# Optimization experiments

Measured on AMD Instinct MI355X. Metric: run time of the kernel, lower is better.

## Reference

```python
import jax, jax.numpy as jnp
import numpy as np

# Constants describing the (equal-length) ragged batch and CRF tag space
B, L = 64, 512                 # 64 sequences of 512 segment-tokens each
C = 1024                       # fuse_embedding_channel
NUM_CLASSES = 5                # real field classes
NUM_TAGS = NUM_CLASSES + 2     # + START + STOP
START, STOP = NUM_CLASSES, NUM_CLASSES + 1
NEG = -10000.0


def setup_inputs() -> dict:
    key = jax.random.key(0)
    k1, k2, k3, k4 = jax.random.split(key, 4)
    fuse_embeddings = jax.random.normal(k1, (B * L, C), jnp.float32)
    label_class = jax.random.randint(k2, (B * L,), 0, NUM_CLASSES)
    # classification head params (Linear C -> NUM_TAGS)
    W = jax.random.normal(k3, (NUM_TAGS, C), jnp.float32) * 0.02
    b = jnp.zeros((NUM_TAGS,), jnp.float32)
    # CRF transition matrix: transitions[next, prev]
    transitions = jax.random.normal(k4, (NUM_TAGS, NUM_TAGS), jnp.float32) * 0.01
    transitions = transitions.at[START, :].set(NEG).at[:, STOP].set(NEG)
    return {"fuse_embeddings": fuse_embeddings, "label_class": label_class,
            "W": W, "b": b, "transitions": transitions}


def _crf_nll_sum(feats, tags, transitions):
    """Sum over batch of (forward_alg score - gold score).
    feats: [B, L, T] emissions, tags: [B, L] int, transitions: [T, T] (next, prev)."""
    # --- forward algorithm (batched log-sum-exp recurrence) ---
    init = jnp.full((B, NUM_TAGS), NEG, feats.dtype).at[:, START].set(0.0)

    def step(fv, emit):
        # fv: [B, prev], emit: [B, next]
        fv_new = jax.nn.logsumexp(fv[:, None, :] + transitions[None, :, :], axis=2) + emit
        return fv_new, None

    fv, _ = jax.lax.scan(step, init, jnp.swapaxes(feats, 0, 1))  # scan over L
    fwd_score = jax.nn.logsumexp(fv + transitions[STOP][None, :], axis=1)  # [B]

    # --- gold sentence score ---
    tags_ext = jnp.concatenate([jnp.full((B, 1), START, tags.dtype), tags], axis=1)
    emit_sc = jnp.take_along_axis(feats, tags[..., None], axis=2)[..., 0].sum(axis=1)
    trans_sc = transitions[tags_ext[:, 1:], tags_ext[:, :-1]].sum(axis=1)
    gold = emit_sc + trans_sc + transitions[STOP, tags[:, -1]]
    return (fwd_score - gold).sum()


def reference(fuse_embeddings, label_class, W, b, transitions):
    # per-token linear projection to tag logits
    pred_class = fuse_embeddings @ W.T + b          # [N, NUM_TAGS]
    feats = pred_class.reshape(B, L, NUM_TAGS)
    tags = label_class.reshape(B, L)
    score = _crf_nll_sum(feats, tags, transitions)
    return (jnp.reshape(score, (1,)), label_class.astype(jnp.int32), pred_class)
```

## Files before the change

### kernel.cpp

```cpp
#include <hip/hip_runtime.h>

#define BSEQ 64
#define LSEQ 512
#define CCH  1024
#define NT   7
#define NC   5
#define NTOK (BSEQ*LSEQ)
#define START_TAG 5
#define STOP_TAG  6
#define NEGV (-10000.0f)
#define GRID_LOGITS 1024

typedef float vfloat4 __attribute__((ext_vector_type(4)));

template<int CTRL, int RMASK, int BMASK>
__device__ __forceinline__ float dpp_add(float x) {
    int y = __builtin_amdgcn_update_dpp(0, __float_as_int(x), CTRL, RMASK, BMASK, true);
    return x + __int_as_float(y);
}
__device__ __forceinline__ float wave_sum(float x) {
    x = dpp_add<0x111, 0xF, 0xF>(x);
    x = dpp_add<0x112, 0xF, 0xF>(x);
    x = dpp_add<0x114, 0xF, 0xF>(x);
    x = dpp_add<0x118, 0xF, 0xF>(x);
    x = dpp_add<0x142, 0xA, 0xF>(x);
    x = dpp_add<0x143, 0xC, 0xF>(x);
    return x;
}

__device__ __forceinline__ float lse5(const float v0, const float v1, const float v2,
                                      const float v3, const float v4) {
    float m = fmaxf(fmaxf(fmaxf(v0, v1), fmaxf(v2, v3)), v4);
    float s = __expf(v0 - m) + __expf(v1 - m) + __expf(v2 - m)
            + __expf(v3 - m) + __expf(v4 - m);
    return m + __logf(s);
}

__global__ __launch_bounds__(256)
void k_logits(const float* __restrict__ X, const float* __restrict__ W,
              const float* __restrict__ bvec, const int* __restrict__ lab,
              float* __restrict__ out)
{
    __shared__ float Wl[NT][CCH];
    __shared__ float bl[NT];
    {
        const vfloat4* W4  = (const vfloat4*)W;
        vfloat4*       Wl4 = (vfloat4*)(&Wl[0][0]);
        for (int i = threadIdx.x; i < NT*CCH/4; i += 256) Wl4[i] = W4[i];
        if (threadIdx.x < NT) bl[threadIdx.x] = bvec[threadIdx.x];
    }
    __syncthreads();

    const int lane = threadIdx.x & 63;
    const int wid  = (blockIdx.x * 256 + threadIdx.x) >> 6;
    const int nw   = (GRID_LOGITS * 256) >> 6;
    float* outP = out + 1 + NTOK;

    vfloat4 xv[2][2][4];

    {
        const size_t r0 = (size_t)wid * 2;
        const vfloat4* x0 = (const vfloat4*)(X + r0 * CCH);
        const vfloat4* x1 = (const vfloat4*)(X + (r0 + 1) * CCH);
        #pragma unroll
        for (int k = 0; k < 4; k++) {
            xv[0][0][k] = __builtin_nontemporal_load(&x0[k*64 + lane]);
            xv[0][1][k] = __builtin_nontemporal_load(&x1[k*64 + lane]);
        }
    }

    #pragma unroll
    for (int it = 0; it < 4; ++it) {
        const int buf = it & 1;
        if (it < 3) {
            const size_t rn = (size_t)(wid + (it + 1) * nw) * 2;
            const vfloat4* x0 = (const vfloat4*)(X + rn * CCH);
            const vfloat4* x1 = (const vfloat4*)(X + (rn + 1) * CCH);
            #pragma unroll
            for (int k = 0; k < 4; k++) {
                xv[buf ^ 1][0][k] = __builtin_nontemporal_load(&x0[k*64 + lane]);
                xv[buf ^ 1][1][k] = __builtin_nontemporal_load(&x1[k*64 + lane]);
            }
        }

        float acc[2][NT];
        #pragma unroll
        for (int r = 0; r < 2; r++)
            #pragma unroll
            for (int t = 0; t < NT; t++) acc[r][t] = 0.0f;

        #pragma unroll
        for (int k = 0; k < 4; k++) {
            const int cb = (k*64 + lane) * 4;
            #pragma unroll
            for (int t = 0; t < NT; t++) {
                const vfloat4 wv = *(const vfloat4*)(&Wl[t][cb]);
                #pragma unroll
                for (int r = 0; r < 2; r++) {
                    acc[r][t] = fmaf(xv[buf][r][k].x, wv.x,
                                fmaf(xv[buf][r][k].y, wv.y,
                                fmaf(xv[buf][r][k].z, wv.z,
                                fmaf(xv[buf][r][k].w, wv.w, acc[r][t]))));
                }
            }
        }

        const size_t base = (size_t)(wid + it * nw) * 2;
        #pragma unroll
        for (int r = 0; r < 2; r++) {
            #pragma unroll
            for (int t = 0; t < NT; t++) {
                float s = wave_sum(acc[r][t]);
                if (lane == 63) outP[(base + r) * NT + t] = s + bl[t];
            }
        }
    }

    for (int i = blockIdx.x * 256 + threadIdx.x; i < NTOK; i += GRID_LOGITS * 256)
        out[1 + i] = (float)lab[i];
    if (blockIdx.x == 0 && threadIdx.x == 0) out[0] = 0.0f;
}

__global__ __launch_bounds__(320)
void k_crf(const float* __restrict__ dout_ro, const int* __restrict__ lab,
           const float* __restrict__ trans, float* __restrict__ score)
{
    __shared__ float E[LSEQ*NT];
    __shared__ float M2[32*25];
    __shared__ float T[49];
    __shared__ float u_sh[NC];
    __shared__ float gred[5];

    const int b   = blockIdx.x;
    const int tid = threadIdx.x;
    const float* feats = dout_ro + 1 + NTOK + (size_t)b * (LSEQ*NT);

    for (int i = tid; i < LSEQ*NT; i += 320) E[i] = feats[i];
    if (tid < 49) T[tid] = trans[tid];
    __syncthreads();

    if (tid < NC) u_sh[tid] = T[tid*NT + START_TAG] + E[tid];

    float g = 0.0f;
    for (int l = tid; l < LSEQ; l += 320) {
        const int t  = lab[b*LSEQ + l];
        const int tp = (l == 0) ? START_TAG : lab[b*LSEQ + l - 1];
        g += E[l*NT + t] + T[t*NT + tp];
    }
    if (tid == 0) g += T[STOP_TAG*NT + lab[b*LSEQ + LSEQ - 1]];
    {
        float gs = wave_sum(g);
        if ((tid & 63) == 63) gred[tid >> 6] = gs;
    }

    float TR[NC*NC];
    #pragma unroll
    for (int j = 0; j < NC; j++)
        #pragma unroll
        for (int k = 0; k < NC; k++) TR[j*NC + k] = T[j*NT + k];

    const int chunk = tid / NC;
    const int basis = tid - chunk * NC;
    float fv[NC];
    #pragma unroll
    for (int j = 0; j < NC; j++) fv[j] = (j == basis) ? 0.0f : NEGV;

    const int l0    = (chunk == 0) ? 1 : chunk * 8;
    const int steps = (chunk == 0) ? 7 : 8;
    for (int s = 0; s < steps; s++) {
        const int l = l0 + s;
        float fn[NC];
        #pragma unroll
        for (int j = 0; j < NC; j++) {
            fn[j] = lse5(fv[0] + TR[j*NC+0], fv[1] + TR[j*NC+1], fv[2] + TR[j*NC+2],
                         fv[3] + TR[j*NC+3], fv[4] + TR[j*NC+4]) + E[l*NT + j];
        }
        #pragma unroll
        for (int j = 0; j < NC; j++) fv[j] = fn[j];
    }
    __syncthreads();
    #pragma unroll
    for (int j = 0; j < NC; j++) E[chunk*25 + basis*NC + j] = fv[j];

    int n = 64, cur = 0;
    while (n > 1) {
        __syncthreads();
        const float* in = (cur == 0) ? (const float*)E : (const float*)M2;
        float*       ob = (cur == 0) ? M2 : E;
        const int half = n >> 1;
        for (int e2 = tid; e2 < half*25; e2 += 320) {
            const int p = e2 / 25, r = e2 - p*25;
            const int i = r / NC, j = r - (r/NC)*NC;
            const float* A  = in + (2*p)*25 + i*NC;
            const float* Bm = in + (2*p + 1)*25 + j;
            ob[p*25 + r] = lse5(A[0] + Bm[0], A[1] + Bm[NC], A[2] + Bm[2*NC],
                                A[3] + Bm[3*NC], A[4] + Bm[4*NC]);
        }
        cur ^= 1; n = half;
    }
    __syncthreads();

    if (tid == 0) {
        float gg = gred[0] + gred[1] + gred[2] + gred[3] + gred[4];
        const float* M = (cur == 0) ? (const float*)E : (const float*)M2;
        float v[NC];
        #pragma unroll
        for (int j = 0; j < NC; j++)
            v[j] = lse5(u_sh[0] + M[0*NC+j], u_sh[1] + M[1*NC+j], u_sh[2] + M[2*NC+j],
                        u_sh[3] + M[3*NC+j], u_sh[4] + M[4*NC+j]);
        float fwd = lse5(v[0] + T[STOP_TAG*NT+0], v[1] + T[STOP_TAG*NT+1],
                         v[2] + T[STOP_TAG*NT+2], v[3] + T[STOP_TAG*NT+3],
                         v[4] + T[STOP_TAG*NT+4]);
        atomicAdd(score, fwd - gg);
    }
}

extern "C" void kernel_launch(void* const* d_in, const int* in_sizes, int n_in,
                              void* d_out, int out_size, void* d_ws, size_t ws_size,
                              hipStream_t stream) {
    const float* X     = (const float*)d_in[0];
    const int*   lab   = (const int*)  d_in[1];
    const float* W     = (const float*)d_in[2];
    const float* bvec  = (const float*)d_in[3];
    const float* trans = (const float*)d_in[4];
    float* out = (float*)d_out;

    k_logits<<<GRID_LOGITS, 256, 0, stream>>>(X, W, bvec, lab, out);
    k_crf<<<BSEQ, 320, 0, stream>>>(out, lab, trans, out);
}
```

Before: 212.1 us.

## Deepen X prefetch to four rows ahead and issue before W staging

Restructures the logits kernel so each wave processes one row per iteration over eight iterations, using a five-slot register ring that keeps four rows of X in flight. The first four rows are loaded before W is staged into shared memory, so global loads overlap the LDS fill and the barrier. Nontemporal loads are replaced with ordinary loads. The deeper prefetch raises register use, which may lower occupancy, and the rows each wave touches are interleaved differently.

```diff
diff --git a/kernel.cpp b/kernel.cpp
--- a/kernel.cpp
+++ b/kernel.cpp
@@ -43,6 +43,20 @@
 {
     __shared__ float Wl[NT][CCH];
     __shared__ float bl[NT];
+
+    const int lane = threadIdx.x & 63;
+    const int wid  = (blockIdx.x * 256 + threadIdx.x) >> 6;
+    const int nw   = (GRID_LOGITS * 256) >> 6;
+
+    vfloat4 xv[5][4];
+
+    #pragma unroll
+    for (int p = 0; p < 4; p++) {
+        const vfloat4* xr = (const vfloat4*)(X + (size_t)(wid + p * nw) * CCH);
+        #pragma unroll
+        for (int k = 0; k < 4; k++) xv[p][k] = xr[k*64 + lane];
+    }
+
     {
         const vfloat4* W4  = (const vfloat4*)W;
         vfloat4*       Wl4 = (vfloat4*)(&Wl[0][0]);
@@ -51,43 +65,21 @@
     }
     __syncthreads();
 
-    const int lane = threadIdx.x & 63;
-    const int wid  = (blockIdx.x * 256 + threadIdx.x) >> 6;
-    const int nw   = (GRID_LOGITS * 256) >> 6;
     float* outP = out + 1 + NTOK;
 
-    vfloat4 xv[2][2][4];
-
-    {
-        const size_t r0 = (size_t)wid * 2;
-        const vfloat4* x0 = (const vfloat4*)(X + r0 * CCH);
-        const vfloat4* x1 = (const vfloat4*)(X + (r0 + 1) * CCH);
-        #pragma unroll
-        for (int k = 0; k < 4; k++) {
-            xv[0][0][k] = __builtin_nontemporal_load(&x0[k*64 + lane]);
-            xv[0][1][k] = __builtin_nontemporal_load(&x1[k*64 + lane]);
-        }
-    }
-
-    #pragma unroll
-    for (int it = 0; it < 4; ++it) {
-        const int buf = it & 1;
-        if (it < 3) {
-            const size_t rn = (size_t)(wid + (it + 1) * nw) * 2;
-            const vfloat4* x0 = (const vfloat4*)(X + rn * CCH);
-            const vfloat4* x1 = (const vfloat4*)(X + (rn + 1) * CCH);
+    #pragma unroll
+    for (int it = 0; it < 8; ++it) {
+        const int buf = it % 5;
+        if (it < 4) {
+            const vfloat4* xr = (const vfloat4*)(X + (size_t)(wid + (it + 4) * nw) * CCH);
+            const int nb = (it + 4) % 5;
             #pragma unroll
-            for (int k = 0; k < 4; k++) {
-                xv[buf ^ 1][0][k] = __builtin_nontemporal_load(&x0[k*64 + lane]);
-                xv[buf ^ 1][1][k] = __builtin_nontemporal_load(&x1[k*64 + lane]);
-            }
-        }
-
-        float acc[2][NT];
-        #pragma unroll
-        for (int r = 0; r < 2; r++)
-            #pragma unroll
-            for (int t = 0; t < NT; t++) acc[r][t] = 0.0f;
+            for (int k = 0; k < 4; k++) xv[nb][k] = xr[k*64 + lane];
+        }
+
+        float acc[NT];
+        #pragma unroll
+        for (int t = 0; t < NT; t++) acc[t] = 0.0f;
 
         #pragma unroll
         for (int k = 0; k < 4; k++) {
@@ -95,24 +87,18 @@
             #pragma unroll
             for (int t = 0; t < NT; t++) {
                 const vfloat4 wv = *(const vfloat4*)(&Wl[t][cb]);
-                #pragma unroll
-                for (int r = 0; r < 2; r++) {
-                    acc[r][t] = fmaf(xv[buf][r][k].x, wv.x,
-                                fmaf(xv[buf][r][k].y, wv.y,
-                                fmaf(xv[buf][r][k].z, wv.z,
-                                fmaf(xv[buf][r][k].w, wv.w, acc[r][t]))));
-                }
+                acc[t] = fmaf(xv[buf][k].x, wv.x,
+                         fmaf(xv[buf][k].y, wv.y,
+                         fmaf(xv[buf][k].z, wv.z,
+                         fmaf(xv[buf][k].w, wv.w, acc[t]))));
             }
         }
 
-        const size_t base = (size_t)(wid + it * nw) * 2;
-        #pragma unroll
-        for (int r = 0; r < 2; r++) {
-            #pragma unroll
-            for (int t = 0; t < NT; t++) {
-                float s = wave_sum(acc[r][t]);
-                if (lane == 63) outP[(base + r) * NT + t] = s + bl[t];
-            }
+        const size_t row = (size_t)(wid + it * nw);
+        #pragma unroll
+        for (int t = 0; t < NT; t++) {
+            float s = wave_sum(acc[t]);
+            if (lane == 63) outP[row * NT + t] = s + bl[t];
         }
     }
 
```

Result: slower. 218.7 us (+3.1%).
